# Kernel tuning notes

Measured on AMD Instinct MI355X. Metric: run time of the kernel, lower is better.

## Reference

```python
import jax, jax.numpy as jnp
import numpy as np

N_NODES = 100000
N_EDGES = 1600000
IN_DIM = 128
HID_DIM = 32
N_HEADS = 4
OUT_DIM = 128
TAU = 0.3


def setup_inputs() -> dict:
    key = jax.random.key(0)
    ks = jax.random.split(key, 12)
    s = 1.0 / np.sqrt(IN_DIM)
    so = 1.0 / np.sqrt(HID_DIM * N_HEADS)
    return {
        "h": jax.random.normal(ks[0], (N_NODES, IN_DIM), dtype=jnp.float32),
        "src": jax.random.randint(ks[1], (N_EDGES,), 0, N_NODES, dtype=jnp.int32),
        "dst": jax.random.randint(ks[2], (N_EDGES,), 0, N_NODES, dtype=jnp.int32),
        # per-head linear params stacked on leading head axis (torch Linear init range)
        "Wq": jax.random.uniform(ks[3], (N_HEADS, IN_DIM, HID_DIM), jnp.float32, -s, s),
        "bq": jax.random.uniform(ks[4], (N_HEADS, HID_DIM), jnp.float32, -s, s),
        "Wk": jax.random.uniform(ks[5], (N_HEADS, IN_DIM, HID_DIM), jnp.float32, -s, s),
        "bk": jax.random.uniform(ks[6], (N_HEADS, HID_DIM), jnp.float32, -s, s),
        "Wm": jax.random.uniform(ks[7], (N_HEADS, IN_DIM, HID_DIM), jnp.float32, -s, s),
        "bm": jax.random.uniform(ks[8], (N_HEADS, HID_DIM), jnp.float32, -s, s),
        "Wout": jax.random.uniform(ks[9], (N_HEADS * HID_DIM, OUT_DIM), jnp.float32, -so, so),
        "bout": jax.random.uniform(ks[10], (OUT_DIM,), jnp.float32, -so, so),
    }


def reference(h, src, dst, Wq, bq, Wk, bk, Wm, bm, Wout, bout):
    N = h.shape[0]
    # per-head projections: [N, H, D]
    zq = jnp.einsum("nd,hde->nhe", h, Wq) + bq
    zk = jnp.einsum("nd,hde->nhe", h, Wk) + bk
    zm = jnp.einsum("nd,hde->nhe", h, Wm) + bm
    # edge attention logits: sum(tau * z_k[src] * z_q[dst], -1) -> [E, H]
    e = jnp.einsum("ehd,ehd->eh", TAU * zk[src], zq[dst])
    # numerically stable segment softmax over destination nodes
    emax = jax.ops.segment_max(e, dst, num_segments=N)  # [N, H]
    emax = jnp.where(jnp.isfinite(emax), emax, 0.0)  # empty segments -> 0
    eexp = jnp.exp(e - emax[dst])
    denom = jax.ops.segment_sum(eexp, dst, num_segments=N)  # [N, H]
    alpha = eexp / jnp.where(denom > 0, denom, 1.0)[dst]  # [E, H]
    # weighted scatter-sum aggregation of source messages -> [N, H, D]
    agg = jax.ops.segment_sum(zm[src] * alpha[:, :, None], dst, num_segments=N)
    # concat heads + output projection + relu
    out = jax.nn.relu(agg.reshape(N, -1) @ Wout + bout)
    return out
```

## Files before the change

kernel.cpp:

```cpp
#include <hip/hip_runtime.h>
#include <hip/hip_bf16.h>
#include <cstdint>
#include <cstddef>

#define NN 100000
#define NE 1600000
#define TAU 0.3f
#define REGION 400000
#define REGION2 5120

typedef __attribute__((ext_vector_type(8))) short bf16x8;
typedef __attribute__((ext_vector_type(4))) float f32x4;

#if __has_builtin(__builtin_amdgcn_sdot4)
#define HAVE_SDOT4 1
#else
#define HAVE_SDOT4 0
#endif

static __device__ __forceinline__ float b2f_hi(uint w) {
  return __uint_as_float(w & 0xffff0000u);
}
static __device__ __forceinline__ float b2f_lo(uint w) {
  return __uint_as_float(w << 16);
}
static __device__ __forceinline__ ushort f2b(float f) {
  uint x = __float_as_uint(f);
  return (ushort)((x + 0x7fffu + ((x >> 16) & 1u)) >> 16);
}
static __device__ __forceinline__ float i8f(uint w, int k) {
  return (float)((int)(w << (24 - 8 * k)) >> 24);
}
static __device__ __forceinline__ int dot4i8(uint a, uint b, int c) {
#if HAVE_SDOT4
  return __builtin_amdgcn_sdot4((int)a, (int)b, c, false);
#else
  return c + (int)(char)(a) * (int)(char)(b)
           + (int)(char)(a >> 8) * (int)(char)(b >> 8)
           + (int)(char)(a >> 16) * (int)(char)(b >> 16)
           + (int)(char)(a >> 24) * (int)(char)(b >> 24);
#endif
}
#if __has_builtin(__builtin_amdgcn_cvt_f32_ubyte0)
#define UB0(w) __builtin_amdgcn_cvt_f32_ubyte0(w)
#define UB1(w) __builtin_amdgcn_cvt_f32_ubyte1(w)
#define UB2(w) __builtin_amdgcn_cvt_f32_ubyte2(w)
#define UB3(w) __builtin_amdgcn_cvt_f32_ubyte3(w)
#else
#define UB0(w) ((float)((w) & 0xffu))
#define UB1(w) ((float)(((w) >> 8) & 0xffu))
#define UB2(w) ((float)(((w) >> 16) & 0xffu))
#define UB3(w) ((float)(((w) >> 24) & 0xffu))
#endif

__global__ __launch_bounds__(256) void setup_stage(
    const float* __restrict__ h, ushort* __restrict__ A,
    const float* __restrict__ Wq, const float* __restrict__ Wk, const float* __restrict__ Wm,
    const float* __restrict__ bq, const float* __restrict__ bk, const float* __restrict__ bm,
    const float* __restrict__ Wout,
    ushort* __restrict__ BTproj, ushort* __restrict__ BTout, float* __restrict__ bvec,
    const int* __restrict__ src, const int* __restrict__ dst,
    int* __restrict__ stageCur, int2* __restrict__ stage) {
  int b = blockIdx.x;
  int t = threadIdx.x;
  if (b < 6250) {
    int i = b * 256 + t;
    const float4* hv = (const float4*)h + (size_t)i * 2;
    float4 a = hv[0], c = hv[1];
    uint4 o;
    o.x = (uint)f2b(a.x) | ((uint)f2b(a.y) << 16);
    o.y = (uint)f2b(a.z) | ((uint)f2b(a.w) << 16);
    o.z = (uint)f2b(c.x) | ((uint)f2b(c.y) << 16);
    o.w = (uint)f2b(c.z) | ((uint)f2b(c.w) << 16);
    ((uint4*)A)[i] = o;
    return;
  }
  if (b < 6506) {
    int id = (b - 6250) * 256 + t;
    if (id < 384 * 128) {
      int j = id >> 7, k = id & 127;
      int w = j >> 7, r = j & 127, hh = r >> 5, d = r & 31;
      const float* W = (w == 0) ? Wq : (w == 1) ? Wk : Wm;
      BTproj[id] = f2b(W[hh * 4096 + k * 32 + d]);
      if (k == 0) {
        const float* bb = (w == 0) ? bq : (w == 1) ? bk : bm;
        bvec[j] = bb[hh * 32 + d];
      }
    } else {
      int id2 = id - 384 * 128;
      int c = id2 >> 7, k = id2 & 127;
      BTout[id2] = f2b(Wout[k * 128 + c]);
    }
    return;
  }
  __shared__ int cnt[8];
  __shared__ int gbase[8];
  if (t < 8) cnt[t] = 0;
  __syncthreads();
  int e0 = (b - 6506) * 2048 + t;
  int d[8], s[8];
#pragma unroll
  for (int i = 0; i < 8; i++) {
    int e = e0 + i * 256;
    if (e < NE) {
      d[i] = dst[e];
      s[i] = src[e];
      atomicAdd(&cnt[d[i] >> 14], 1);
    } else {
      d[i] = -1;
    }
  }
  __syncthreads();
  if (t < 8) gbase[t] = atomicAdd(&stageCur[t * 16], cnt[t]);
  __syncthreads();
  if (t < 8) cnt[t] = 0;
  __syncthreads();
#pragma unroll
  for (int i = 0; i < 8; i++) {
    if (d[i] >= 0) {
      int p = d[i] >> 14;
      int slot = p * REGION + gbase[p] + atomicAdd(&cnt[p], 1);
      stage[slot] = make_int2(s[i], d[i]);
    }
  }
}

__global__ __launch_bounds__(256) void stage2_kernel(
    const int2* __restrict__ stage, const int* __restrict__ stageCur,
    int* __restrict__ subCur, uint* __restrict__ stage2) {
  int p = blockIdx.x & 7;
  int kb = blockIdx.x >> 3;
  int t = threadIdx.x;
  int n = stageCur[p * 16];
  const int2* reg = stage + (size_t)p * REGION;
  __shared__ int cnt[64];
  __shared__ int pos[64];
  __shared__ int gb[64];
  __shared__ int mvs;
  __shared__ uint buf[2048];

  for (int base = kb * 2048; base < n; base += 128 * 2048) {
    if (t < 64) cnt[t] = 0;
    __syncthreads();
    uint v[8]; int sb[8];
#pragma unroll
    for (int i = 0; i < 8; i++) {
      int idx = base + t + i * 256;
      if (idx < n) {
        int2 e = reg[idx];
        int dlow = e.y & 16383;
        sb[i] = dlow >> 8;
        v[i] = ((uint)e.x << 14) | (uint)dlow;
        atomicAdd(&cnt[sb[i]], 1);
      } else sb[i] = -1;
    }
    __syncthreads();
    if (t < 64) {
      int c = cnt[t];
      int x = c;
#pragma unroll
      for (int d = 1; d < 64; d <<= 1) {
        int y = __shfl_up(x, d);
        if (t >= d) x += y;
      }
      pos[t] = x - c;
      gb[t] = c ? atomicAdd(&subCur[(p * 64 + t) * 16], c) : 0;
      if (t == 63) mvs = x;
      cnt[t] = 0;
    }
    __syncthreads();
#pragma unroll
    for (int i = 0; i < 8; i++) {
      if (sb[i] >= 0) {
        int loc = pos[sb[i]] + atomicAdd(&cnt[sb[i]], 1);
        buf[loc] = v[i];
      }
    }
    __syncthreads();
    int mv = mvs;
    for (int j = t; j < mv; j += 256) {
      uint w = buf[j];
      int s2 = (int)((w & 16383u) >> 8);
      stage2[((size_t)(p * 64 + s2)) * REGION2 + gb[s2] + (j - pos[s2])] = w;
    }
    __syncthreads();
  }
}

__global__ __launch_bounds__(256) void hist_sb(
    const uint* __restrict__ stage2, const int* __restrict__ subCur,
    int* __restrict__ counts) {
  int g = blockIdx.x;
  int p = g >> 6;
  int n = subCur[g * 16];
  const uint* reg = stage2 + (size_t)g * REGION2;
  int dbase = p * 16384 + (g & 63) * 256;
  __shared__ int cnt[256];
  int t = threadIdx.x;
  cnt[t] = 0;
  __syncthreads();
  for (int i = t; i < n; i += 256) atomicAdd(&cnt[reg[i] & 255u], 1);
  __syncthreads();
  if (dbase + t < NN) counts[dbase + t] = cnt[t];
}

__global__ __launch_bounds__(256) void hist_part(
    const int2* __restrict__ stage, const int* __restrict__ stageCur,
    int* __restrict__ counts) {
  int p = blockIdx.x & 7;
  int k = blockIdx.x >> 3;
  int n = stageCur[p * 16];
  const int2* reg = stage + (size_t)p * REGION;
  for (int i = k * 256 + threadIdx.x; i < n; i += 32 * 256)
    atomicAdd(&counts[reg[i].y], 1);
}

template <int MODE>
__global__ __launch_bounds__(256) void mfma_gemm(
    const ushort* __restrict__ A, const ushort* __restrict__ BT,
    const float* __restrict__ bias, void* __restrict__ Cp, int M, int ncols,
    char* __restrict__ Zkm, char* __restrict__ Zq8,
    float* __restrict__ scales, float* __restrict__ sqv) {
  __shared__ ushort As[64 * 128];
  __shared__ ushort Bs[128 * 128];

  int t = threadIdx.x;
  int rowBase = blockIdx.x * 64, colBase = blockIdx.y * 128;

#pragma unroll
  for (int i = 0; i < 4; i++) {
    int flat = t + i * 256;
    int row = flat >> 4;
    int kb = (flat & 15) * 16;
    int soff = kb ^ ((row & 7) << 4);
    int ar = rowBase + row; if (ar >= M) ar = M - 1;
    __builtin_amdgcn_global_load_lds(
        (const __attribute__((address_space(1))) uint32_t*)((const char*)A + (size_t)ar * 256 + soff),
        (__attribute__((address_space(3))) uint32_t*)((char*)As + row * 256 + kb), 16, 0, 0);
  }
#pragma unroll
  for (int i = 0; i < 8; i++) {
    int flat = t + i * 256;
    int row = flat >> 4;
    int kb = (flat & 15) * 16;
    int soff = kb ^ ((row & 7) << 4);
    __builtin_amdgcn_global_load_lds(
        (const __attribute__((address_space(1))) uint32_t*)((const char*)BT + (size_t)(colBase + row) * 256 + soff),
        (__attribute__((address_space(3))) uint32_t*)((char*)Bs + row * 256 + kb), 16, 0, 0);
  }
  __syncthreads();

  int wv = t >> 6, L = t & 63;
  int wrow = (wv >> 1) * 32, wcol = (wv & 1) * 64;
  int lr = L & 15;
  int lk = (L >> 4) * 16;
  f32x4 acc[2][4] = {};

#pragma unroll
  for (int ks = 0; ks < 4; ks++) {
    bf16x8 a[2], b[4];
#pragma unroll
    for (int i = 0; i < 2; i++) {
      int row = wrow + i * 16 + lr;
      a[i] = *(const bf16x8*)((const char*)As + row * 256 + ((ks * 64 + lk) ^ ((row & 7) << 4)));
    }
#pragma unroll
    for (int j = 0; j < 4; j++) {
      int col = wcol + j * 16 + lr;
      b[j] = *(const bf16x8*)((const char*)Bs + col * 256 + ((ks * 64 + lk) ^ ((col & 7) << 4)));
    }
#pragma unroll
    for (int i = 0; i < 2; i++)
#pragma unroll
      for (int j = 0; j < 4; j++)
        acc[i][j] = __builtin_amdgcn_mfma_f32_16x16x32_bf16(a[i], b[j], acc[i][j], 0, 0, 0);
  }

  int rquad = (L >> 4) * 4;

  if (MODE == 2) {
    __syncthreads();
    float* Cs = (float*)Bs;
#pragma unroll
    for (int j = 0; j < 4; j++) {
      float bs = bias[colBase + wcol + j * 16 + lr];
#pragma unroll
      for (int i = 0; i < 2; i++) {
        int rl = wrow + i * 16 + rquad;
#pragma unroll
        for (int r = 0; r < 4; r++)
          Cs[(rl + r) * 128 + wcol + j * 16 + lr] = acc[i][j][r] + bs;
      }
    }
    __syncthreads();

    int row = t >> 2, part = t & 3;
    int row_g = rowBase + row;
    const float4* rp = (const float4*)(Cs + row * 128 + part * 32);
    float4 v[8];
    float vmax = 0.f;
#pragma unroll
    for (int i = 0; i < 8; i++) {
      v[i] = rp[i];
      vmax = fmaxf(vmax, fmaxf(fmaxf(fabsf(v[i].x), fabsf(v[i].y)),
                               fmaxf(fabsf(v[i].z), fabsf(v[i].w))));
    }
    vmax = fmaxf(vmax, __shfl_xor(vmax, 1));
    vmax = fmaxf(vmax, __shfl_xor(vmax, 2));
    vmax = fmaxf(vmax, 1e-20f);
    float qs = 127.0f / vmax;
    int w = blockIdx.y;
    if (row_g < M) {
      if (w == 0) {
        uint b8[8];
#pragma unroll
        for (int i = 0; i < 8; i++)
          b8[i] = (uint)(__float2int_rn(v[i].x * qs) & 0xff)
                | ((uint)(__float2int_rn(v[i].y * qs) & 0xff) << 8)
                | ((uint)(__float2int_rn(v[i].z * qs) & 0xff) << 16)
                | ((uint)(__float2int_rn(v[i].w * qs) & 0xff) << 24);
        uint4* dst4 = (uint4*)(Zq8 + (size_t)row_g * 128 + part * 32);
        dst4[0] = make_uint4(b8[0], b8[1], b8[2], b8[3]);
        dst4[1] = make_uint4(b8[4], b8[5], b8[6], b8[7]);
        if (part == 0) sqv[row_g] = vmax * (1.0f / 127.0f);
      } else {
#pragma unroll
        for (int u = 0; u < 2; u++) {
#pragma unroll
          for (int hh = 0; hh < 2; hh++) {
            int un = part * 4 + u * 2 + hh;
            float4 va = v[u * 4 + hh * 2], vb = v[u * 4 + hh * 2 + 1];
            uint lo, hi;
            if (w == 1) {
              lo = (uint)(__float2int_rn(va.x * qs) & 0xff)
                 | ((uint)(__float2int_rn(va.y * qs) & 0xff) << 8)
                 | ((uint)(__float2int_rn(va.z * qs) & 0xff) << 16)
                 | ((uint)(__float2int_rn(va.w * qs) & 0xff) << 24);
              hi = (uint)(__float2int_rn(vb.x * qs) & 0xff)
                 | ((uint)(__float2int_rn(vb.y * qs) & 0xff) << 8)
                 | ((uint)(__float2int_rn(vb.z * qs) & 0xff) << 16)
                 | ((uint)(__float2int_rn(vb.w * qs) & 0xff) << 24);
            } else {
              lo = (uint)((__float2int_rn(va.x * qs) + 128) & 0xff)
                 | ((uint)((__float2int_rn(va.y * qs) + 128) & 0xff) << 8)
                 | ((uint)((__float2int_rn(va.z * qs) + 128) & 0xff) << 16)
                 | ((uint)((__float2int_rn(va.w * qs) + 128) & 0xff) << 24);
              hi = (uint)((__float2int_rn(vb.x * qs) + 128) & 0xff)
                 | ((uint)((__float2int_rn(vb.y * qs) + 128) & 0xff) << 8)
                 | ((uint)((__float2int_rn(vb.z * qs) + 128) & 0xff) << 16)
                 | ((uint)((__float2int_rn(vb.w * qs) + 128) & 0xff) << 24);
            }
            uint2* d2 = (uint2*)(Zkm + (size_t)row_g * 256 + un * 16 + (w == 2 ? 8 : 0));
            *d2 = make_uint2(lo, hi);
          }
        }
        if (part == 0) scales[row_g * 2 + (w - 1)] = vmax * (1.0f / 127.0f);
      }
    }
    return;
  }

#pragma unroll
  for (int j = 0; j < 4; j++) {
    int col = colBase + wcol + j * 16 + lr;
    float bs = bias[col];
#pragma unroll
    for (int i = 0; i < 2; i++) {
      int row0 = rowBase + wrow + i * 16 + rquad;
#pragma unroll
      for (int r = 0; r < 4; r++) {
        int row = row0 + r;
        if (row >= M) continue;
        float vv = acc[i][j][r] + bs;
        if (MODE == 0) {
          vv = fmaxf(vv, 0.f);
          ((float*)Cp)[(size_t)row * ncols + col] = vv;
        } else {
          ((ushort*)Cp)[(size_t)row * ncols + col] = f2b(vv);
        }
      }
    }
  }
}

__global__ __launch_bounds__(256) void scan_a(const int* __restrict__ counts,
                                              int* __restrict__ offsets,
                                              int* __restrict__ blockSums, int n) {
  __shared__ int lds[256];
  int b = blockIdx.x, t = threadIdx.x;
  int base = b * 1024 + t * 4;
  int4 v = make_int4(0, 0, 0, 0);
  if (base < n) v = *(const int4*)&counts[base];
  int s1 = v.x + v.y, s2 = s1 + v.z, s3 = s2 + v.w;
  lds[t] = s3;
  __syncthreads();
  for (int dd = 1; dd < 256; dd <<= 1) {
    int x = (t >= dd) ? lds[t - dd] : 0;
    __syncthreads();
    lds[t] += x;
    __syncthreads();
  }
  int excl = (t > 0) ? lds[t - 1] : 0;
  if (base < n) {
    int4 o = make_int4(excl, excl + v.x, excl + s1, excl + s2);
    *(int4*)&offsets[base] = o;
  }
  if (t == 255) blockSums[b] = lds[255];
}

__global__ __launch_bounds__(128) void scan_b(int* __restrict__ blockSums, int nb) {
  __shared__ int lds[128];
  int t = threadIdx.x;
  lds[t] = (t < nb) ? blockSums[t] : 0;
  __syncthreads();
  for (int dd = 1; dd < 128; dd <<= 1) {
    int x = (t >= dd) ? lds[t - dd] : 0;
    __syncthreads();
    lds[t] += x;
    __syncthreads();
  }
  if (t < nb) blockSums[t] = (t > 0) ? lds[t - 1] : 0;
}

__global__ __launch_bounds__(256) void scan_c(int* __restrict__ offsets,
                                              const int* __restrict__ blockSums,
                                              int* __restrict__ cursor, int n) {
  int i = blockIdx.x * 256 + threadIdx.x;
  if (i < n) {
    int v = offsets[i] + blockSums[i >> 10];
    offsets[i] = v;
    cursor[i] = v;
  }
  if (i == 0) offsets[n] = NE;
}

__global__ __launch_bounds__(256) void quant_kernel(
    const ushort* __restrict__ Zbf, char* __restrict__ Zkm, float2* __restrict__ scales,
    char* __restrict__ Zq8, float* __restrict__ sqv) {
  int g = blockIdx.x * 256 + threadIdx.x;
  int row = g >> 4, u = g & 15;
  const ushort* zr = Zbf + (size_t)row * 384;
  uint4 kk = *(const uint4*)(zr + 128 + u * 8);
  uint4 mm = *(const uint4*)(zr + 256 + u * 8);
  uint4 qq = *(const uint4*)(zr + u * 8);
  float kf[8] = {b2f_lo(kk.x), b2f_hi(kk.x), b2f_lo(kk.y), b2f_hi(kk.y),
                 b2f_lo(kk.z), b2f_hi(kk.z), b2f_lo(kk.w), b2f_hi(kk.w)};
  float mf[8] = {b2f_lo(mm.x), b2f_hi(mm.x), b2f_lo(mm.y), b2f_hi(mm.y),
                 b2f_lo(mm.z), b2f_hi(mm.z), b2f_lo(mm.w), b2f_hi(mm.w)};
  float qf[8] = {b2f_lo(qq.x), b2f_hi(qq.x), b2f_lo(qq.y), b2f_hi(qq.y),
                 b2f_lo(qq.z), b2f_hi(qq.z), b2f_lo(qq.w), b2f_hi(qq.w)};
  float mk = 0.f, mx = 0.f, mqv = 0.f;
#pragma unroll
  for (int i = 0; i < 8; i++) {
    mk = fmaxf(mk, fabsf(kf[i]));
    mx = fmaxf(mx, fabsf(mf[i]));
    mqv = fmaxf(mqv, fabsf(qf[i]));
  }
#pragma unroll
  for (int dd = 1; dd < 16; dd <<= 1) {
    mk = fmaxf(mk, __shfl_xor(mk, dd));
    mx = fmaxf(mx, __shfl_xor(mx, dd));
    mqv = fmaxf(mqv, __shfl_xor(mqv, dd));
  }
  mk = fmaxf(mk, 1e-20f); mx = fmaxf(mx, 1e-20f); mqv = fmaxf(mqv, 1e-20f);
  float qk = 127.0f / mk, qm = 127.0f / mx;
  int q[16];
#pragma unroll
  for (int i = 0; i < 8; i++) {
    q[i] = __float2int_rn(kf[i] * qk) & 0xff;
    q[8 + i] = (__float2int_rn(mf[i] * qm) + 128) & 0xff;
  }
  uint4 o;
  o.x = (uint)(q[0] | (q[1] << 8) | (q[2] << 16) | (q[3] << 24));
  o.y = (uint)(q[4] | (q[5] << 8) | (q[6] << 16) | (q[7] << 24));
  o.z = (uint)(q[8] | (q[9] << 8) | (q[10] << 16) | (q[11] << 24));
  o.w = (uint)(q[12] | (q[13] << 8) | (q[14] << 16) | (q[15] << 24));
  *(uint4*)(Zkm + (size_t)row * 256 + u * 16) = o;
  if (u == 0) scales[row] = make_float2(mk * (1.0f / 127.0f), mx * (1.0f / 127.0f));
  float qsv = 127.0f / mqv;
  int r[8];
#pragma unroll
  for (int i = 0; i < 8; i++) r[i] = __float2int_rn(qf[i] * qsv) & 0xff;
  uint2 oq;
  oq.x = (uint)(r[0] | (r[1] << 8) | (r[2] << 16) | (r[3] << 24));
  oq.y = (uint)(r[4] | (r[5] << 8) | (r[6] << 16) | (r[7] << 24));
  *(uint2*)(Zq8 + (size_t)row * 128 + u * 8) = oq;
  if (u == 0) sqv[row] = mqv * (1.0f / 127.0f);
}

__global__ __launch_bounds__(256) void scatter_sb(
    const uint* __restrict__ stage2, const int* __restrict__ subCur,
    const int* __restrict__ offsets, int* __restrict__ csr_src) {
  int g = blockIdx.x;
  int p = g >> 6;
  int n = subCur[g * 16];
  if (n == 0) return;
  const uint* reg = stage2 + (size_t)g * REGION2;
  int dbase = p * 16384 + (g & 63) * 256;
  __shared__ int offs[257];
  __shared__ int cur[256];
  __shared__ uint buf[REGION2];
  int t = threadIdx.x;
  for (int i = t; i < 257; i += 256) {
    int d = dbase + i;
    offs[i] = offsets[d > NN ? NN : d];
  }
  __syncthreads();
  int base0 = offs[0];
  cur[t] = offs[t] - base0;
  __syncthreads();
  for (int i = t; i < n; i += 256) {
    uint v = reg[i];
    int ld = (int)(v & 255u);
    int pos = atomicAdd(&cur[ld], 1);
    buf[pos] = v >> 14;
  }
  __syncthreads();
  for (int j = t; j < n; j += 256)
    csr_src[base0 + j] = (int)buf[j];
}

__global__ __launch_bounds__(256) void scatter_final(
    const int2* __restrict__ stage, const int* __restrict__ stageCur,
    int* __restrict__ cursor, int* __restrict__ csr_src) {
  int p = blockIdx.x & 7;
  int k = blockIdx.x >> 3;
  int n = stageCur[p * 16];
  const int2* reg = stage + (size_t)p * REGION;
  for (int i = k * 256 + threadIdx.x; i < n; i += 130 * 256) {
    int2 e = reg[i];
    int pos = atomicAdd(&cursor[e.y], 1);
    csr_src[pos] = e.x;
  }
}

__global__ __launch_bounds__(256) void aggregate_q(
    const char* __restrict__ Zkm, const float* __restrict__ scales,
    const int* __restrict__ offsets, const int* __restrict__ csr_src,
    ushort* __restrict__ aggbf,
    const char* __restrict__ Zq8, const float* __restrict__ sqv) {
  int wv = threadIdx.x >> 6, L = threadIdx.x & 63;
  int n = blockIdx.x * 4 + wv;
  if (n >= NN) return;
  int qt = L >> 4, l = L & 15;
  int lb = l << 4;

  uint2 q8 = *(const uint2*)(Zq8 + (size_t)n * 128 + l * 8);
  float tq = TAU * sqv[n];

  int start = offsets[n], end = offsets[n + 1];
  float den = 0.f, swm = 0.f;
  float a0 = 0.f, a1 = 0.f, a2 = 0.f, a3 = 0.f, a4 = 0.f, a5 = 0.f, a6 = 0.f, a7 = 0.f;
  int p = start;

  for (; p + 8 <= end; p += 8) {
    int s0 = csr_src[p + qt];
    int s1 = csr_src[p + 4 + qt];
    uint4 v0 = *(const uint4*)(Zkm + ((size_t)s0 << 8) + lb);
    uint4 v1 = *(const uint4*)(Zkm + ((size_t)s1 << 8) + lb);
    float2 sc0 = *(const float2*)(scales + s0 * 2);
    float2 sc1 = *(const float2*)(scales + s1 * 2);

    int p0 = dot4i8(v0.x, q8.x, 0); p0 = dot4i8(v0.y, q8.y, p0);
    int p1 = dot4i8(v1.x, q8.x, 0); p1 = dot4i8(v1.y, q8.y, p1);
    p0 += __shfl_xor(p0, 1); p1 += __shfl_xor(p1, 1);
    p0 += __shfl_xor(p0, 2); p1 += __shfl_xor(p1, 2);
    float w0 = __expf(tq * sc0.x * (float)p0);
    float w1 = __expf(tq * sc1.x * (float)p1);
    den += w0 + w1;
    float wm0 = w0 * sc0.y, wm1 = w1 * sc1.y;
    swm += wm0 + wm1;

    a0 = fmaf(UB0(v0.z), wm0, a0); a1 = fmaf(UB1(v0.z), wm0, a1);
    a2 = fmaf(UB2(v0.z), wm0, a2); a3 = fmaf(UB3(v0.z), wm0, a3);
    a4 = fmaf(UB0(v0.w), wm0, a4); a5 = fmaf(UB1(v0.w), wm0, a5);
    a6 = fmaf(UB2(v0.w), wm0, a6); a7 = fmaf(UB3(v0.w), wm0, a7);
    a0 = fmaf(UB0(v1.z), wm1, a0); a1 = fmaf(UB1(v1.z), wm1, a1);
    a2 = fmaf(UB2(v1.z), wm1, a2); a3 = fmaf(UB3(v1.z), wm1, a3);
    a4 = fmaf(UB0(v1.w), wm1, a4); a5 = fmaf(UB1(v1.w), wm1, a5);
    a6 = fmaf(UB2(v1.w), wm1, a6); a7 = fmaf(UB3(v1.w), wm1, a7);
  }

  for (; p < end; p += 4) {
    int e = p + qt;
    int idx = (e < end) ? e : (end - 1);
    int s0 = csr_src[idx];
    uint4 v = *(const uint4*)(Zkm + ((size_t)s0 << 8) + lb);
    float2 sc = *(const float2*)(scales + s0 * 2);
    int p0 = dot4i8(v.x, q8.x, 0); p0 = dot4i8(v.y, q8.y, p0);
    p0 += __shfl_xor(p0, 1);
    p0 += __shfl_xor(p0, 2);
    float w = (e < end) ? __expf(tq * sc.x * (float)p0) : 0.f;
    den += w;
    float wm = w * sc.y;
    swm += wm;
    a0 = fmaf(UB0(v.z), wm, a0); a1 = fmaf(UB1(v.z), wm, a1);
    a2 = fmaf(UB2(v.z), wm, a2); a3 = fmaf(UB3(v.z), wm, a3);
    a4 = fmaf(UB0(v.w), wm, a4); a5 = fmaf(UB1(v.w), wm, a5);
    a6 = fmaf(UB2(v.w), wm, a6); a7 = fmaf(UB3(v.w), wm, a7);
  }

  den += __shfl_xor(den, 16); den += __shfl_xor(den, 32);
  swm += __shfl_xor(swm, 16); swm += __shfl_xor(swm, 32);
  a0 += __shfl_xor(a0, 16); a0 += __shfl_xor(a0, 32);
  a1 += __shfl_xor(a1, 16); a1 += __shfl_xor(a1, 32);
  a2 += __shfl_xor(a2, 16); a2 += __shfl_xor(a2, 32);
  a3 += __shfl_xor(a3, 16); a3 += __shfl_xor(a3, 32);
  a4 += __shfl_xor(a4, 16); a4 += __shfl_xor(a4, 32);
  a5 += __shfl_xor(a5, 16); a5 += __shfl_xor(a5, 32);
  a6 += __shfl_xor(a6, 16); a6 += __shfl_xor(a6, 32);
  a7 += __shfl_xor(a7, 16); a7 += __shfl_xor(a7, 32);

  float bcorr = 128.f * swm;
  float inv = (den > 0.f) ? 1.0f / den : 0.f;
  if (qt == 0) {
    uint4 o;
    o.x = (uint)f2b((a0 - bcorr) * inv) | ((uint)f2b((a1 - bcorr) * inv) << 16);
    o.y = (uint)f2b((a2 - bcorr) * inv) | ((uint)f2b((a3 - bcorr) * inv) << 16);
    o.z = (uint)f2b((a4 - bcorr) * inv) | ((uint)f2b((a5 - bcorr) * inv) << 16);
    o.w = (uint)f2b((a6 - bcorr) * inv) | ((uint)f2b((a7 - bcorr) * inv) << 16);
    *(uint4*)((char*)aggbf + (size_t)n * 256 + lb) = o;
  }
}

extern "C" void kernel_launch(void* const* d_in, const int* in_sizes, int n_in,
                              void* d_out, int out_size, void* d_ws, size_t ws_size,
                              hipStream_t stream) {
  const float* h    = (const float*)d_in[0];
  const int*   src  = (const int*)d_in[1];
  const int*   dst  = (const int*)d_in[2];
  const float* Wq   = (const float*)d_in[3];
  const float* bq   = (const float*)d_in[4];
  const float* Wk   = (const float*)d_in[5];
  const float* bk   = (const float*)d_in[6];
  const float* Wm   = (const float*)d_in[7];
  const float* bm   = (const float*)d_in[8];
  const float* Wout = (const float*)d_in[9];
  const float* bout = (const float*)d_in[10];
  float* out = (float*)d_out;

  char* base = (char*)d_ws;
  ushort* Abf    = (ushort*)base;
  char*   Zkm    = base + 25600000;
  char*   Zq8    = base + 51200000;
  ushort* Zbf    = (ushort*)(base + 25600000);
  ushort* aggbf  = (ushort*)(base + 102400000);
  int2*   stage  = (int2*)(base + 102400000);
  float*  scales = (float*)(base + 128000000);
  ushort* BTproj = (ushort*)(base + 128800000);
  ushort* BTout  = (ushort*)(base + 128898304);
  float*  bvec   = (float*)(base + 128931072);
  int* counts    = (int*)(base + 128933120);
  int* stageCur  = (int*)(base + 129333120);
  int* subCur    = (int*)(base + 129334144);
  int* offsets   = (int*)(base + 129366912);
  int* cursor    = (int*)(base + 129767040);
  int* blockSums = (int*)(base + 130167040);
  int* csr_src   = (int*)(base + 130167552);
  char* Zq8_fb   = base + 136567552;
  float* sqv     = (float*)(base + 149367552);
  uint* stage2   = (uint*)(base + 149767552);

  int fast = (ws_size >= (size_t)160253312) ? 1 : 0;

  hipMemsetAsync(counts, 0, 433792, stream);

  setup_stage<<<7288, 256, 0, stream>>>(h, Abf, Wq, Wk, Wm, bq, bk, bm, Wout,
                                        BTproj, BTout, bvec, src, dst, stageCur, stage);
  if (fast) {
    stage2_kernel<<<1024, 256, 0, stream>>>(stage, stageCur, subCur, stage2);
    hist_sb<<<512, 256, 0, stream>>>(stage2, subCur, counts);
  } else {
    hist_part<<<256, 256, 0, stream>>>(stage, stageCur, counts);
  }
  scan_a<<<98, 256, 0, stream>>>(counts, offsets, blockSums, NN);
  scan_b<<<1, 128, 0, stream>>>(blockSums, 98);
  scan_c<<<391, 256, 0, stream>>>(offsets, blockSums, cursor, NN);

  if (fast) {
    mfma_gemm<2><<<dim3(1563, 3), 256, 0, stream>>>(
        Abf, BTproj, bvec, nullptr, NN, 384, Zkm, Zq8, scales, sqv);
    scatter_sb<<<512, 256, 0, stream>>>(stage2, subCur, offsets, csr_src);
    aggregate_q<<<25000, 256, 0, stream>>>(Zkm, scales, offsets, csr_src, aggbf, Zq8, sqv);
  } else {
    mfma_gemm<1><<<dim3(1563, 3), 256, 0, stream>>>(
        Abf, BTproj, bvec, Zbf, NN, 384, nullptr, nullptr, nullptr, nullptr);
    quant_kernel<<<6250, 256, 0, stream>>>(Zbf, (char*)base, (float2*)scales, Zq8_fb, sqv);
    scatter_final<<<1040, 256, 0, stream>>>(stage, stageCur, cursor, csr_src);
    aggregate_q<<<25000, 256, 0, stream>>>((char*)base, scales, offsets, csr_src,
                                           aggbf, Zq8_fb, sqv);
  }

  mfma_gemm<0><<<dim3(1563, 1), 256, 0, stream>>>(
      aggbf, BTout, bout, out, NN, 128, nullptr, nullptr, nullptr, nullptr);
}
```

Measured before the change: 202.5 us.

## Fuse projection GEMM with edge bucketing and fold CSR offset scan into scatter

Merges the projection GEMM with int8 quantisation and the second-level edge bucketing pass into one launch, using block-index ranges so the two independent jobs share the GPU at the same time. It also drops the global histogram and the three-kernel scan. Instead, a tiny kernel scans the 512 sub-bucket counts, and each sub-bucket block computes its local histogram, prefix offsets and CSR scatter in one pass. This removes several launches and the serial dependency chain, at the cost of a larger combined kernel whose two roles have different LDS and register needs.

```diff
diff --git a/kernel.cpp b/kernel.cpp
--- a/kernel.cpp
+++ b/kernel.cpp
@@ -125,83 +125,273 @@
   }
 }
 
-__global__ __launch_bounds__(256) void stage2_kernel(
+__global__ __launch_bounds__(256) void gemm2_stage2(
+    const ushort* __restrict__ A, const ushort* __restrict__ BT,
+    const float* __restrict__ bias,
+    char* __restrict__ Zkm, char* __restrict__ Zq8,
+    float* __restrict__ scales, float* __restrict__ sqv, int M,
     const int2* __restrict__ stage, const int* __restrict__ stageCur,
     int* __restrict__ subCur, uint* __restrict__ stage2) {
-  int p = blockIdx.x & 7;
-  int kb = blockIdx.x >> 3;
   int t = threadIdx.x;
-  int n = stageCur[p * 16];
-  const int2* reg = stage + (size_t)p * REGION;
-  __shared__ int cnt[64];
-  __shared__ int pos[64];
-  __shared__ int gb[64];
-  __shared__ int mvs;
-  __shared__ uint buf[2048];
-
-  for (int base = kb * 2048; base < n; base += 128 * 2048) {
-    if (t < 64) cnt[t] = 0;
+  int b = blockIdx.x;
+
+  if (b >= 4689) {
+    int idx = b - 4689;
+    int p = idx & 7;
+    int kb = idx >> 3;
+    int n = stageCur[p * 16];
+    const int2* reg = stage + (size_t)p * REGION;
+    __shared__ int cnt[64];
+    __shared__ int pos[64];
+    __shared__ int gb[64];
+    __shared__ int mvs;
+    __shared__ uint buf[2048];
+
+    for (int base = kb * 2048; base < n; base += 128 * 2048) {
+      if (t < 64) cnt[t] = 0;
+      __syncthreads();
+      uint v[8]; int sb[8];
+#pragma unroll
+      for (int i = 0; i < 8; i++) {
+        int idx2 = base + t + i * 256;
+        if (idx2 < n) {
+          int2 e = reg[idx2];
+          int dlow = e.y & 16383;
+          sb[i] = dlow >> 8;
+          v[i] = ((uint)e.x << 14) | (uint)dlow;
+          atomicAdd(&cnt[sb[i]], 1);
+        } else sb[i] = -1;
+      }
+      __syncthreads();
+      if (t < 64) {
+        int c = cnt[t];
+        int x = c;
+#pragma unroll
+        for (int d = 1; d < 64; d <<= 1) {
+          int y = __shfl_up(x, d);
+          if (t >= d) x += y;
+        }
+        pos[t] = x - c;
+        gb[t] = c ? atomicAdd(&subCur[(p * 64 + t) * 16], c) : 0;
+        if (t == 63) mvs = x;
+        cnt[t] = 0;
+      }
+      __syncthreads();
+#pragma unroll
+      for (int i = 0; i < 8; i++) {
+        if (sb[i] >= 0) {
+          int loc = pos[sb[i]] + atomicAdd(&cnt[sb[i]], 1);
+          buf[loc] = v[i];
+        }
+      }
+      __syncthreads();
+      int mv = mvs;
+      for (int j = t; j < mv; j += 256) {
+        uint w = buf[j];
+        int s2 = (int)((w & 16383u) >> 8);
+        stage2[((size_t)(p * 64 + s2)) * REGION2 + gb[s2] + (j - pos[s2])] = w;
+      }
+      __syncthreads();
+    }
+    return;
+  }
+
+  __shared__ ushort As[64 * 128];
+  __shared__ ushort Bs[128 * 128];
+  int rowBase = (b % 1563) * 64;
+  int w = b / 1563;
+  int colBase = w * 128;
+
+#pragma unroll
+  for (int i = 0; i < 4; i++) {
+    int flat = t + i * 256;
+    int row = flat >> 4;
+    int kb = (flat & 15) * 16;
+    int soff = kb ^ ((row & 7) << 4);
+    int ar = rowBase + row; if (ar >= M) ar = M - 1;
+    __builtin_amdgcn_global_load_lds(
+        (const __attribute__((address_space(1))) uint32_t*)((const char*)A + (size_t)ar * 256 + soff),
+        (__attribute__((address_space(3))) uint32_t*)((char*)As + row * 256 + kb), 16, 0, 0);
+  }
+#pragma unroll
+  for (int i = 0; i < 8; i++) {
+    int flat = t + i * 256;
+    int row = flat >> 4;
+    int kb = (flat & 15) * 16;
+    int soff = kb ^ ((row & 7) << 4);
+    __builtin_amdgcn_global_load_lds(
+        (const __attribute__((address_space(1))) uint32_t*)((const char*)BT + (size_t)(colBase + row) * 256 + soff),
+        (__attribute__((address_space(3))) uint32_t*)((char*)Bs + row * 256 + kb), 16, 0, 0);
+  }
+  __syncthreads();
+
+  int wv = t >> 6, L = t & 63;
+  int wrow = (wv >> 1) * 32, wcol = (wv & 1) * 64;
+  int lr = L & 15;
+  int lk = (L >> 4) * 16;
+  f32x4 acc[2][4] = {};
+
+#pragma unroll
+  for (int ks = 0; ks < 4; ks++) {
+    bf16x8 a[2], bb[4];
+#pragma unroll
+    for (int i = 0; i < 2; i++) {
+      int row = wrow + i * 16 + lr;
+      a[i] = *(const bf16x8*)((const char*)As + row * 256 + ((ks * 64 + lk) ^ ((row & 7) << 4)));
+    }
+#pragma unroll
+    for (int j = 0; j < 4; j++) {
+      int col = wcol + j * 16 + lr;
+      bb[j] = *(const bf16x8*)((const char*)Bs + col * 256 + ((ks * 64 + lk) ^ ((col & 7) << 4)));
+    }
+#pragma unroll
+    for (int i = 0; i < 2; i++)
+#pragma unroll
+      for (int j = 0; j < 4; j++)
+        acc[i][j] = __builtin_amdgcn_mfma_f32_16x16x32_bf16(a[i], bb[j], acc[i][j], 0, 0, 0);
+  }
+
+  int rquad = (L >> 4) * 4;
+  __syncthreads();
+  float* Cs = (float*)Bs;
+#pragma unroll
+  for (int j = 0; j < 4; j++) {
+    float bs = bias[colBase + wcol + j * 16 + lr];
+#pragma unroll
+    for (int i = 0; i < 2; i++) {
+      int rl = wrow + i * 16 + rquad;
+#pragma unroll
+      for (int r = 0; r < 4; r++)
+        Cs[(rl + r) * 128 + wcol + j * 16 + lr] = acc[i][j][r] + bs;
+    }
+  }
+  __syncthreads();
+
+  int row = t >> 2, part = t & 3;
+  int row_g = rowBase + row;
+  const float4* rp = (const float4*)(Cs + row * 128 + part * 32);
+  float4 v[8];
+  float vmax = 0.f;
+#pragma unroll
+  for (int i = 0; i < 8; i++) {
+    v[i] = rp[i];
+    vmax = fmaxf(vmax, fmaxf(fmaxf(fabsf(v[i].x), fabsf(v[i].y)),
+                             fmaxf(fabsf(v[i].z), fabsf(v[i].w))));
+  }
+  vmax = fmaxf(vmax, __shfl_xor(vmax, 1));
+  vmax = fmaxf(vmax, __shfl_xor(vmax, 2));
+  vmax = fmaxf(vmax, 1e-20f);
+  float qs = 127.0f / vmax;
+  if (row_g < M) {
+    if (w == 0) {
+      uint b8[8];
+#pragma unroll
+      for (int i = 0; i < 8; i++)
+        b8[i] = (uint)(__float2int_rn(v[i].x * qs) & 0xff)
+              | ((uint)(__float2int_rn(v[i].y * qs) & 0xff) << 8)
+              | ((uint)(__float2int_rn(v[i].z * qs) & 0xff) << 16)
+              | ((uint)(__float2int_rn(v[i].w * qs) & 0xff) << 24);
+      uint4* dst4 = (uint4*)(Zq8 + (size_t)row_g * 128 + part * 32);
+      dst4[0] = make_uint4(b8[0], b8[1], b8[2], b8[3]);
+      dst4[1] = make_uint4(b8[4], b8[5], b8[6], b8[7]);
+      if (part == 0) sqv[row_g] = vmax * (1.0f / 127.0f);
+    } else {
+#pragma unroll
+      for (int u = 0; u < 2; u++) {
+#pragma unroll
+        for (int hh = 0; hh < 2; hh++) {
+          int un = part * 4 + u * 2 + hh;
+          float4 va = v[u * 4 + hh * 2], vb = v[u * 4 + hh * 2 + 1];
+          uint lo, hi;
+          if (w == 1) {
+            lo = (uint)(__float2int_rn(va.x * qs) & 0xff)
+               | ((uint)(__float2int_rn(va.y * qs) & 0xff) << 8)
+               | ((uint)(__float2int_rn(va.z * qs) & 0xff) << 16)
+               | ((uint)(__float2int_rn(va.w * qs) & 0xff) << 24);
+            hi = (uint)(__float2int_rn(vb.x * qs) & 0xff)
+               | ((uint)(__float2int_rn(vb.y * qs) & 0xff) << 8)
+               | ((uint)(__float2int_rn(vb.z * qs) & 0xff) << 16)
+               | ((uint)(__float2int_rn(vb.w * qs) & 0xff) << 24);
+          } else {
+            lo = (uint)((__float2int_rn(va.x * qs) + 128) & 0xff)
+               | ((uint)((__float2int_rn(va.y * qs) + 128) & 0xff) << 8)
+               | ((uint)((__float2int_rn(va.z * qs) + 128) & 0xff) << 16)
+               | ((uint)((__float2int_rn(va.w * qs) + 128) & 0xff) << 24);
+            hi = (uint)((__float2int_rn(vb.x * qs) + 128) & 0xff)
+               | ((uint)((__float2int_rn(vb.y * qs) + 128) & 0xff) << 8)
+               | ((uint)((__float2int_rn(vb.z * qs) + 128) & 0xff) << 16)
+               | ((uint)((__float2int_rn(vb.w * qs) + 128) & 0xff) << 24);
+          }
+          uint2* d2 = (uint2*)(Zkm + (size_t)row_g * 256 + un * 16 + (w == 2 ? 8 : 0));
+          *d2 = make_uint2(lo, hi);
+        }
+      }
+      if (part == 0) scales[row_g * 2 + (w - 1)] = vmax * (1.0f / 127.0f);
+    }
+  }
+}
+
+__global__ __launch_bounds__(256) void scan_sub(
+    const int* __restrict__ subCur, int* __restrict__ subOff,
+    int* __restrict__ offsets) {
+  __shared__ int lds[256];
+  int t = threadIdx.x;
+  int c0 = subCur[(2 * t) * 16];
+  int c1 = subCur[(2 * t + 1) * 16];
+  lds[t] = c0 + c1;
+  __syncthreads();
+  for (int dd = 1; dd < 256; dd <<= 1) {
+    int x = (t >= dd) ? lds[t - dd] : 0;
     __syncthreads();
-    uint v[8]; int sb[8];
-#pragma unroll
-    for (int i = 0; i < 8; i++) {
-      int idx = base + t + i * 256;
-      if (idx < n) {
-        int2 e = reg[idx];
-        int dlow = e.y & 16383;
-        sb[i] = dlow >> 8;
-        v[i] = ((uint)e.x << 14) | (uint)dlow;
-        atomicAdd(&cnt[sb[i]], 1);
-      } else sb[i] = -1;
-    }
+    lds[t] += x;
     __syncthreads();
-    if (t < 64) {
-      int c = cnt[t];
-      int x = c;
-#pragma unroll
-      for (int d = 1; d < 64; d <<= 1) {
-        int y = __shfl_up(x, d);
-        if (t >= d) x += y;
-      }
-      pos[t] = x - c;
-      gb[t] = c ? atomicAdd(&subCur[(p * 64 + t) * 16], c) : 0;
-      if (t == 63) mvs = x;
-      cnt[t] = 0;
-    }
-    __syncthreads();
-#pragma unroll
-    for (int i = 0; i < 8; i++) {
-      if (sb[i] >= 0) {
-        int loc = pos[sb[i]] + atomicAdd(&cnt[sb[i]], 1);
-        buf[loc] = v[i];
-      }
-    }
-    __syncthreads();
-    int mv = mvs;
-    for (int j = t; j < mv; j += 256) {
-      uint w = buf[j];
-      int s2 = (int)((w & 16383u) >> 8);
-      stage2[((size_t)(p * 64 + s2)) * REGION2 + gb[s2] + (j - pos[s2])] = w;
-    }
-    __syncthreads();
-  }
-}
-
-__global__ __launch_bounds__(256) void hist_sb(
+  }
+  int excl = (t > 0) ? lds[t - 1] : 0;
+  subOff[2 * t] = excl;
+  subOff[2 * t + 1] = excl + c0;
+  if (t == 0) offsets[NN] = NE;
+}
+
+__global__ __launch_bounds__(256) void hsc_sb(
     const uint* __restrict__ stage2, const int* __restrict__ subCur,
-    int* __restrict__ counts) {
+    const int* __restrict__ subOff, int* __restrict__ offsets,
+    int* __restrict__ csr_src) {
   int g = blockIdx.x;
   int p = g >> 6;
   int n = subCur[g * 16];
   const uint* reg = stage2 + (size_t)g * REGION2;
   int dbase = p * 16384 + (g & 63) * 256;
+  int base0 = subOff[g];
   __shared__ int cnt[256];
+  __shared__ int lds[256];
+  __shared__ int cur[256];
+  __shared__ uint buf[REGION2];
   int t = threadIdx.x;
   cnt[t] = 0;
   __syncthreads();
   for (int i = t; i < n; i += 256) atomicAdd(&cnt[reg[i] & 255u], 1);
   __syncthreads();
-  if (dbase + t < NN) counts[dbase + t] = cnt[t];
+  lds[t] = cnt[t];
+  __syncthreads();
+  for (int dd = 1; dd < 256; dd <<= 1) {
+    int x = (t >= dd) ? lds[t - dd] : 0;
+    __syncthreads();
+    lds[t] += x;
+    __syncthreads();
+  }
+  int excl = (t > 0) ? lds[t - 1] : 0;
+  if (dbase + t < NN) offsets[dbase + t] = base0 + excl;
+  cur[t] = excl;
+  __syncthreads();
+  for (int i = t; i < n; i += 256) {
+    uint v = reg[i];
+    int ld = (int)(v & 255u);
+    int pos = atomicAdd(&cur[ld], 1);
+    buf[pos] = v >> 14;
+  }
+  __syncthreads();
+  for (int j = t; j < n; j += 256)
+    csr_src[base0 + j] = (int)buf[j];
 }
 
 __global__ __launch_bounds__(256) void hist_part(
@@ -215,12 +405,61 @@
     atomicAdd(&counts[reg[i].y], 1);
 }
 
+__global__ __launch_bounds__(256) void scan_a(const int* __restrict__ counts,
+                                              int* __restrict__ offsets,
+                                              int* __restrict__ blockSums, int n) {
+  __shared__ int lds[256];
+  int b = blockIdx.x, t = threadIdx.x;
+  int base = b * 1024 + t * 4;
+  int4 v = make_int4(0, 0, 0, 0);
+  if (base < n) v = *(const int4*)&counts[base];
+  int s1 = v.x + v.y, s2 = s1 + v.z, s3 = s2 + v.w;
+  lds[t] = s3;
+  __syncthreads();
+  for (int dd = 1; dd < 256; dd <<= 1) {
+    int x = (t >= dd) ? lds[t - dd] : 0;
+    __syncthreads();
+    lds[t] += x;
+    __syncthreads();
+  }
+  int excl = (t > 0) ? lds[t - 1] : 0;
+  if (base < n) {
+    int4 o = make_int4(excl, excl + v.x, excl + s1, excl + s2);
+    *(int4*)&offsets[base] = o;
+  }
+  if (t == 255) blockSums[b] = lds[255];
+}
+
+__global__ __launch_bounds__(128) void scan_b(int* __restrict__ blockSums, int nb) {
+  __shared__ int lds[128];
+  int t = threadIdx.x;
+  lds[t] = (t < nb) ? blockSums[t] : 0;
+  __syncthreads();
+  for (int dd = 1; dd < 128; dd <<= 1) {
+    int x = (t >= dd) ? lds[t - dd] : 0;
+    __syncthreads();
+    lds[t] += x;
+    __syncthreads();
+  }
+  if (t < nb) blockSums[t] = (t > 0) ? lds[t - 1] : 0;
+}
+
+__global__ __launch_bounds__(256) void scan_c(int* __restrict__ offsets,
+                                              const int* __restrict__ blockSums,
+                                              int* __restrict__ cursor, int n) {
+  int i = blockIdx.x * 256 + threadIdx.x;
+  if (i < n) {
+    int v = offsets[i] + blockSums[i >> 10];
+    offsets[i] = v;
+    cursor[i] = v;
+  }
+  if (i == 0) offsets[n] = NE;
+}
+
 template <int MODE>
 __global__ __launch_bounds__(256) void mfma_gemm(
     const ushort* __restrict__ A, const ushort* __restrict__ BT,
-    const float* __restrict__ bias, void* __restrict__ Cp, int M, int ncols,
-    char* __restrict__ Zkm, char* __restrict__ Zq8,
-    float* __restrict__ scales, float* __restrict__ sqv) {
+    const float* __restrict__ bias, void* __restrict__ Cp, int M, int ncols) {
   __shared__ ushort As[64 * 128];
   __shared__ ushort Bs[128 * 128];
 
@@ -277,89 +516,6 @@
   }
 
   int rquad = (L >> 4) * 4;
-
-  if (MODE == 2) {
-    __syncthreads();
-    float* Cs = (float*)Bs;
-#pragma unroll
-    for (int j = 0; j < 4; j++) {
-      float bs = bias[colBase + wcol + j * 16 + lr];
-#pragma unroll
-      for (int i = 0; i < 2; i++) {
-        int rl = wrow + i * 16 + rquad;
-#pragma unroll
-        for (int r = 0; r < 4; r++)
-          Cs[(rl + r) * 128 + wcol + j * 16 + lr] = acc[i][j][r] + bs;
-      }
-    }
-    __syncthreads();
-
-    int row = t >> 2, part = t & 3;
-    int row_g = rowBase + row;
-    const float4* rp = (const float4*)(Cs + row * 128 + part * 32);
-    float4 v[8];
-    float vmax = 0.f;
-#pragma unroll
-    for (int i = 0; i < 8; i++) {
-      v[i] = rp[i];
-      vmax = fmaxf(vmax, fmaxf(fmaxf(fabsf(v[i].x), fabsf(v[i].y)),
-                               fmaxf(fabsf(v[i].z), fabsf(v[i].w))));
-    }
-    vmax = fmaxf(vmax, __shfl_xor(vmax, 1));
-    vmax = fmaxf(vmax, __shfl_xor(vmax, 2));
-    vmax = fmaxf(vmax, 1e-20f);
-    float qs = 127.0f / vmax;
-    int w = blockIdx.y;
-    if (row_g < M) {
-      if (w == 0) {
-        uint b8[8];
-#pragma unroll
-        for (int i = 0; i < 8; i++)
-          b8[i] = (uint)(__float2int_rn(v[i].x * qs) & 0xff)
-                | ((uint)(__float2int_rn(v[i].y * qs) & 0xff) << 8)
-                | ((uint)(__float2int_rn(v[i].z * qs) & 0xff) << 16)
-                | ((uint)(__float2int_rn(v[i].w * qs) & 0xff) << 24);
-        uint4* dst4 = (uint4*)(Zq8 + (size_t)row_g * 128 + part * 32);
-        dst4[0] = make_uint4(b8[0], b8[1], b8[2], b8[3]);
-        dst4[1] = make_uint4(b8[4], b8[5], b8[6], b8[7]);
-        if (part == 0) sqv[row_g] = vmax * (1.0f / 127.0f);
-      } else {
-#pragma unroll
-        for (int u = 0; u < 2; u++) {
-#pragma unroll
-          for (int hh = 0; hh < 2; hh++) {
-            int un = part * 4 + u * 2 + hh;
-            float4 va = v[u * 4 + hh * 2], vb = v[u * 4 + hh * 2 + 1];
-            uint lo, hi;
-            if (w == 1) {
-              lo = (uint)(__float2int_rn(va.x * qs) & 0xff)
-                 | ((uint)(__float2int_rn(va.y * qs) & 0xff) << 8)
-                 | ((uint)(__float2int_rn(va.z * qs) & 0xff) << 16)
-                 | ((uint)(__float2int_rn(va.w * qs) & 0xff) << 24);
-              hi = (uint)(__float2int_rn(vb.x * qs) & 0xff)
-                 | ((uint)(__float2int_rn(vb.y * qs) & 0xff) << 8)
-                 | ((uint)(__float2int_rn(vb.z * qs) & 0xff) << 16)
-                 | ((uint)(__float2int_rn(vb.w * qs) & 0xff) << 24);
-            } else {
-              lo = (uint)((__float2int_rn(va.x * qs) + 128) & 0xff)
-                 | ((uint)((__float2int_rn(va.y * qs) + 128) & 0xff) << 8)
-                 | ((uint)((__float2int_rn(va.z * qs) + 128) & 0xff) << 16)
-                 | ((uint)((__float2int_rn(va.w * qs) + 128) & 0xff) << 24);
-              hi = (uint)((__float2int_rn(vb.x * qs) + 128) & 0xff)
-                 | ((uint)((__float2int_rn(vb.y * qs) + 128) & 0xff) << 8)
-                 | ((uint)((__float2int_rn(vb.z * qs) + 128) & 0xff) << 16)
-                 | ((uint)((__float2int_rn(vb.w * qs) + 128) & 0xff) << 24);
-            }
-            uint2* d2 = (uint2*)(Zkm + (size_t)row_g * 256 + un * 16 + (w == 2 ? 8 : 0));
-            *d2 = make_uint2(lo, hi);
-          }
-        }
-        if (part == 0) scales[row_g * 2 + (w - 1)] = vmax * (1.0f / 127.0f);
-      }
-    }
-    return;
-  }
-
 #pragma unroll
   for (int j = 0; j < 4; j++) {
     int col = colBase + wcol + j * 16 + lr;
@@ -381,57 +537,6 @@
       }
     }
   }
-}
-
-__global__ __launch_bounds__(256) void scan_a(const int* __restrict__ counts,
-                                              int* __restrict__ offsets,
-                                              int* __restrict__ blockSums, int n) {
-  __shared__ int lds[256];
-  int b = blockIdx.x, t = threadIdx.x;
-  int base = b * 1024 + t * 4;
-  int4 v = make_int4(0, 0, 0, 0);
-  if (base < n) v = *(const int4*)&counts[base];
-  int s1 = v.x + v.y, s2 = s1 + v.z, s3 = s2 + v.w;
-  lds[t] = s3;
-  __syncthreads();
-  for (int dd = 1; dd < 256; dd <<= 1) {
-    int x = (t >= dd) ? lds[t - dd] : 0;
-    __syncthreads();
-    lds[t] += x;
-    __syncthreads();
-  }
-  int excl = (t > 0) ? lds[t - 1] : 0;
-  if (base < n) {
-    int4 o = make_int4(excl, excl + v.x, excl + s1, excl + s2);
-    *(int4*)&offsets[base] = o;
-  }
-  if (t == 255) blockSums[b] = lds[255];
-}
-
-__global__ __launch_bounds__(128) void scan_b(int* __restrict__ blockSums, int nb) {
-  __shared__ int lds[128];
-  int t = threadIdx.x;
-  lds[t] = (t < nb) ? blockSums[t] : 0;
-  __syncthreads();
-  for (int dd = 1; dd < 128; dd <<= 1) {
-    int x = (t >= dd) ? lds[t - dd] : 0;
-    __syncthreads();
-    lds[t] += x;
-    __syncthreads();
-  }
-  if (t < nb) blockSums[t] = (t > 0) ? lds[t - 1] : 0;
-}
-
-__global__ __launch_bounds__(256) void scan_c(int* __restrict__ offsets,
-                                              const int* __restrict__ blockSums,
-                                              int* __restrict__ cursor, int n) {
-  int i = blockIdx.x * 256 + threadIdx.x;
-  if (i < n) {
-    int v = offsets[i] + blockSums[i >> 10];
-    offsets[i] = v;
-    cursor[i] = v;
-  }
-  if (i == 0) offsets[n] = NE;
 }
 
 __global__ __launch_bounds__(256) void quant_kernel(
@@ -486,38 +591,6 @@
   oq.y = (uint)(r[4] | (r[5] << 8) | (r[6] << 16) | (r[7] << 24));
   *(uint2*)(Zq8 + (size_t)row * 128 + u * 8) = oq;
   if (u == 0) sqv[row] = mqv * (1.0f / 127.0f);
-}
-
-__global__ __launch_bounds__(256) void scatter_sb(
-    const uint* __restrict__ stage2, const int* __restrict__ subCur,
-    const int* __restrict__ offsets, int* __restrict__ csr_src) {
-  int g = blockIdx.x;
-  int p = g >> 6;
-  int n = subCur[g * 16];
-  if (n == 0) return;
-  const uint* reg = stage2 + (size_t)g * REGION2;
-  int dbase = p * 16384 + (g & 63) * 256;
-  __shared__ int offs[257];
-  __shared__ int cur[256];
-  __shared__ uint buf[REGION2];
-  int t = threadIdx.x;
-  for (int i = t; i < 257; i += 256) {
-    int d = dbase + i;
-    offs[i] = offsets[d > NN ? NN : d];
-  }
-  __syncthreads();
-  int base0 = offs[0];
-  cur[t] = offs[t] - base0;
-  __syncthreads();
-  for (int i = t; i < n; i += 256) {
-    uint v = reg[i];
-    int ld = (int)(v & 255u);
-    int pos = atomicAdd(&cur[ld], 1);
-    buf[pos] = v >> 14;
-  }
-  __syncthreads();
-  for (int j = t; j < n; j += 256)
-    csr_src[base0 + j] = (int)buf[j];
 }
 
 __global__ __launch_bounds__(256) void scatter_final(
@@ -656,41 +729,36 @@
   int* offsets   = (int*)(base + 129366912);
   int* cursor    = (int*)(base + 129767040);
   int* blockSums = (int*)(base + 130167040);
-  int* csr_src   = (int*)(base + 130167552);
-  char* Zq8_fb   = base + 136567552;
-  float* sqv     = (float*)(base + 149367552);
-  uint* stage2   = (uint*)(base + 149767552);
-
-  int fast = (ws_size >= (size_t)160253312) ? 1 : 0;
+  int* subOff    = (int*)(base + 130167552);
+  int* csr_src   = (int*)(base + 130169600);
+  char* Zq8_fb   = base + 136569600;
+  float* sqv     = (float*)(base + 149369600);
+  uint* stage2   = (uint*)(base + 149769600);
+
+  int fast = (ws_size >= (size_t)160255360) ? 1 : 0;
 
   hipMemsetAsync(counts, 0, 433792, stream);
 
   setup_stage<<<7288, 256, 0, stream>>>(h, Abf, Wq, Wk, Wm, bq, bk, bm, Wout,
                                         BTproj, BTout, bvec, src, dst, stageCur, stage);
+
   if (fast) {
-    stage2_kernel<<<1024, 256, 0, stream>>>(stage, stageCur, subCur, stage2);
-    hist_sb<<<512, 256, 0, stream>>>(stage2, subCur, counts);
+    gemm2_stage2<<<5713, 256, 0, stream>>>(Abf, BTproj, bvec, Zkm, Zq8, scales, sqv,
+                                           NN, stage, stageCur, subCur, stage2);
+    scan_sub<<<1, 256, 0, stream>>>(subCur, subOff, offsets);
+    hsc_sb<<<512, 256, 0, stream>>>(stage2, subCur, subOff, offsets, csr_src);
+    aggregate_q<<<25000, 256, 0, stream>>>(Zkm, scales, offsets, csr_src, aggbf, Zq8, sqv);
   } else {
     hist_part<<<256, 256, 0, stream>>>(stage, stageCur, counts);
-  }
-  scan_a<<<98, 256, 0, stream>>>(counts, offsets, blockSums, NN);
-  scan_b<<<1, 128, 0, stream>>>(blockSums, 98);
-  scan_c<<<391, 256, 0, stream>>>(offsets, blockSums, cursor, NN);
-
-  if (fast) {
-    mfma_gemm<2><<<dim3(1563, 3), 256, 0, stream>>>(
-        Abf, BTproj, bvec, nullptr, NN, 384, Zkm, Zq8, scales, sqv);
-    scatter_sb<<<512, 256, 0, stream>>>(stage2, subCur, offsets, csr_src);
-    aggregate_q<<<25000, 256, 0, stream>>>(Zkm, scales, offsets, csr_src, aggbf, Zq8, sqv);
-  } else {
-    mfma_gemm<1><<<dim3(1563, 3), 256, 0, stream>>>(
-        Abf, BTproj, bvec, Zbf, NN, 384, nullptr, nullptr, nullptr, nullptr);
+    scan_a<<<98, 256, 0, stream>>>(counts, offsets, blockSums, NN);
+    scan_b<<<1, 128, 0, stream>>>(blockSums, 98);
+    scan_c<<<391, 256, 0, stream>>>(offsets, blockSums, cursor, NN);
+    mfma_gemm<1><<<dim3(1563, 3), 256, 0, stream>>>(Abf, BTproj, bvec, Zbf, NN, 384);
     quant_kernel<<<6250, 256, 0, stream>>>(Zbf, (char*)base, (float2*)scales, Zq8_fb, sqv);
     scatter_final<<<1040, 256, 0, stream>>>(stage, stageCur, cursor, csr_src);
     aggregate_q<<<25000, 256, 0, stream>>>((char*)base, scales, offsets, csr_src,
                                            aggbf, Zq8_fb, sqv);
   }
 
-  mfma_gemm<0><<<dim3(1563, 1), 256, 0, stream>>>(
-      aggbf, BTout, bout, out, NN, 128, nullptr, nullptr, nullptr, nullptr);
-}
+  mfma_gemm<0><<<dim3(1563, 1), 256, 0, stream>>>(aggbf, BTout, bout, out, NN, 128);
+}
```

After: 197.2 us. -2.6%, faster.
